# Optimization experiments

Measured on AMD Instinct MI355X. Metric: run time of the kernel, lower is better.

The kernel has to match this reference:

```python
import jax, jax.numpy as jnp
import numpy as np

DIM_MODEL = 512
DIM_HEAD = 64


def setup_inputs() -> dict:
    key = jax.random.key(0)
    ks = jax.random.split(key, 7)
    B, S = 4, 4096
    x = jax.random.normal(ks[0], (B, S, DIM_MODEL), dtype=jnp.float32)
    mask = jnp.ones((B, 1, S), dtype=jnp.int32)
    # torch Linear init: U(-1/sqrt(fan_in), 1/sqrt(fan_in)); stored as (in, out) for x @ W
    bound = 1.0 / np.sqrt(DIM_MODEL)
    Wq = jax.random.uniform(ks[1], (DIM_MODEL, DIM_HEAD), minval=-bound, maxval=bound, dtype=jnp.float32)
    bq = jax.random.uniform(ks[2], (DIM_HEAD,), minval=-bound, maxval=bound, dtype=jnp.float32)
    Wk = jax.random.uniform(ks[3], (DIM_MODEL, DIM_HEAD), minval=-bound, maxval=bound, dtype=jnp.float32)
    bk = jax.random.uniform(ks[4], (DIM_HEAD,), minval=-bound, maxval=bound, dtype=jnp.float32)
    Wv = jax.random.uniform(ks[5], (DIM_MODEL, DIM_HEAD), minval=-bound, maxval=bound, dtype=jnp.float32)
    bv = jax.random.uniform(ks[6], (DIM_HEAD,), minval=-bound, maxval=bound, dtype=jnp.float32)
    return {"x": x, "mask": mask, "Wq": Wq, "bq": bq, "Wk": Wk, "bk": bk, "Wv": Wv, "bv": bv}


def reference(x, mask, Wq, bq, Wk, bk, Wv, bv):
    # single-head QKV projection
    q = x @ Wq + bq  # (B, S, Dh)
    k = x @ Wk + bk
    v = x @ Wv + bv
    dot_scale = jnp.sqrt(jnp.float32(DIM_HEAD))
    # explicit O(S^2) score matrix, softmax over keys
    scores = jnp.einsum("bqd,bkd->bqk", q, k) / dot_scale  # (B, S, S)
    attn = jax.nn.softmax(scores, axis=-1)
    # faithful to source: mask applied AFTER softmax with -inf fill
    attn = jnp.where(mask == 0, jnp.float32(-jnp.inf), attn)
    return jnp.einsum("bqk,bkd->bqd", attn, v)  # (B, S, Dh)
```

## Files before the change

### kernel.cpp

```cpp
#include <hip/hip_runtime.h>
#include <hip/hip_bf16.h>

typedef _Float16 half8v __attribute__((ext_vector_type(8)));
typedef _Float16 half4v __attribute__((ext_vector_type(4)));
typedef _Float16 half2v __attribute__((ext_vector_type(2)));
typedef __fp16   fp16x2 __attribute__((ext_vector_type(2)));
typedef __attribute__((ext_vector_type(4))) float floatx4;

#define LOG2E_OVER_8 0.18033688011112042f


__device__ __forceinline__ void gload_lds16(const void* g, void* l) {
    __builtin_amdgcn_global_load_lds(
        (const __attribute__((address_space(1))) void*)(unsigned long long)g,
        (__attribute__((address_space(3))) void*)(unsigned)(unsigned long long)l,
        16, 0, 0);
}

__global__ __launch_bounds__(256) void wtrans_k(const float* __restrict__ Wq,
                                                const float* __restrict__ Wk,
                                                const float* __restrict__ Wv,
                                                _Float16* __restrict__ Wt) {
    int idx = blockIdx.x * 256 + threadIdx.x;
    int p = idx >> 15, rem = idx & 32767;
    int k = rem >> 6;
    int n = rem & 63;
    const float* W = (p == 0) ? Wq : ((p == 1) ? Wk : Wv);
    int ctg = p * 4 + (n >> 4), m = n & 15;
    int kc = k >> 5, quad = (k >> 3) & 3, j = k & 7;
    Wt[(((ctg << 4) + kc) * 64 + (quad << 4) + m) * 8 + j] = (_Float16)W[k * 64 + n];
}

#define XS_STRIDE 536
__global__ __launch_bounds__(256) void proj_k(const float* __restrict__ x,
                                              const _Float16* __restrict__ Wt,
                                              const float* __restrict__ bq,
                                              const float* __restrict__ bk,
                                              const float* __restrict__ bv,
                                              _Float16* __restrict__ Qh,
                                              _Float16* __restrict__ Kh,
                                              _Float16* __restrict__ Vh) {
    __shared__ _Float16 xs[2][16 * XS_STRIDE];

    int tid = threadIdx.x, l = tid & 63, wv = tid >> 6;
    int m = l & 15, quad = l >> 4;
    int row0 = blockIdx.x * 32;

#pragma unroll
    for (int s = 0; s < 2; s++)
#pragma unroll
        for (int i = 0; i < 8; i++) {
            int idx = tid + i * 256;
            int row = idx >> 7, c4 = idx & 127;
            float4 v = *(const float4*)(x + (row0 + s * 16 + row) * 512 + c4 * 4);
            union { half2v h[2]; uint2 u; } cv;
            cv.h[0][0] = (_Float16)v.x; cv.h[0][1] = (_Float16)v.y;
            cv.h[1][0] = (_Float16)v.z; cv.h[1][1] = (_Float16)v.w;
            *(uint2*)(xs[s] + row * XS_STRIDE + c4 * 4) = cv.u;
        }
    __syncthreads();

    const _Float16* arow0 = xs[0] + m * XS_STRIDE + quad * 8;
    const _Float16* arow1 = xs[1] + m * XS_STRIDE + quad * 8;

    floatx4 acc[2][3];
#pragma unroll
    for (int s = 0; s < 2; s++)
#pragma unroll
        for (int i = 0; i < 3; i++) acc[s][i] = (floatx4)(0.f);

#pragma unroll 4
    for (int kc = 0; kc < 16; kc++) {
        half8v a0 = *(const half8v*)(arow0 + kc * 32);
        half8v a1 = *(const half8v*)(arow1 + kc * 32);
#pragma unroll
        for (int ct = 0; ct < 3; ct++) {
            int ctg = wv * 3 + ct;
            half8v b = *(const half8v*)(Wt + (((ctg << 4) + kc) * 64 + l) * 8);
            acc[0][ct] = __builtin_amdgcn_mfma_f32_16x16x32_f16(a0, b, acc[0][ct], 0, 0, 0);
            acc[1][ct] = __builtin_amdgcn_mfma_f32_16x16x32_f16(a1, b, acc[1][ct], 0, 0, 0);
        }
    }

#pragma unroll
    for (int s = 0; s < 2; s++) {
        int rowb = row0 + s * 16;
#pragma unroll
        for (int ct = 0; ct < 3; ct++) {
            int ctg = wv * 3 + ct;
            int col = ctg * 16 + m;
            float bias = (ctg < 4) ? bq[col] : ((ctg < 8) ? bk[col - 64] : bv[col - 128]);
            if (ctg < 8) {
                _Float16* dst = (ctg < 4) ? Qh : Kh;
                float scl = (ctg < 4) ? LOG2E_OVER_8 : 1.0f;
                int dd = (ctg & 3) * 16 + m;
                int c = dd >> 5, quadQ = (dd >> 3) & 3, j = dd & 7;
#pragma unroll
                for (int r = 0; r < 4; r++) {
                    int row = rowb + quad * 4 + r;
                    int chunk = ((row >> 4) << 1) + c;
                    dst[(chunk * 64 + quadQ * 16 + (row & 15)) * 8 + j] =
                        (_Float16)((acc[s][ct][r] + bias) * scl);
                }
            } else {
                int dt = ctg - 8;
                int t64 = rowb >> 6, ktp = (rowb >> 5) & 1, half = (rowb >> 4) & 1;
                int chunk = t64 * 8 + dt * 2 + ktp;
                union { _Float16 h[4]; unsigned long long u; } pk;
#pragma unroll
                for (int r = 0; r < 4; r++) pk.h[r] = (_Float16)(acc[s][ct][r] + bias);
                *(unsigned long long*)(Vh + (chunk * 64 + quad * 16 + m) * 8 + half * 4) = pk.u;
            }
        }
    }
}

template <int NT>
__global__ __launch_bounds__(256) void attn_k(const _Float16* __restrict__ Qh,
                                              const _Float16* __restrict__ Kh,
                                              const _Float16* __restrict__ Vh,
                                              const int* __restrict__ mask,
                                              _Float16* __restrict__ Np,
                                              float* __restrict__ Dp,
                                              int gshift) {
    __shared__ __align__(16) uint4 stage_lds[2][1024];

    int tid = threadIdx.x, l = tid & 63, wv = tid >> 6;
    int m = l & 15, quad = l >> 4;
    int bid = blockIdx.x;
    int grp = bid & ((1 << gshift) - 1), qblk = bid >> gshift;
    int os = grp >> 2, b = grp & 3;
    int q0 = qblk * 128 + wv * 32;

    const int* maskb = mask + b * 4096 + os * (NT * 64);
    int az = 0;
#pragma unroll
    for (int i = 0; i < NT; i++) az |= (maskb[l + i * 64] == 0);
    const bool hasz = __any(az);

    int qt_g = (b * 4096 + q0) >> 4;
    half8v qf[2][2];
#pragma unroll
    for (int qt = 0; qt < 2; qt++)
#pragma unroll
        for (int c = 0; c < 2; c++)
            qf[qt][c] = *(const half8v*)(Qh + (((qt_g + qt) * 2 + c) * 64 + l) * 8);

    half8v ones8;
#pragma unroll
    for (int i = 0; i < 8; i++) ones8[i] = (_Float16)1.0f;

    int tb0 = (b * 64 + os * NT) * 512;
    const uint4* kh4 = (const uint4*)Kh + tb0;
    const uint4* vh4 = (const uint4*)Vh + tb0;

    floatx4 oacc[2][4];
#pragma unroll
    for (int qt = 0; qt < 2; qt++)
#pragma unroll
        for (int dt = 0; dt < 4; dt++) oacc[qt][dt] = (floatx4)(0.f);
    floatx4 oden[2] = {(floatx4)(0.f), (floatx4)(0.f)};

#pragma unroll
    for (int i = 0; i < 2; i++) {
        int idx = wv * 128 + i * 64 + l;
        gload_lds16(kh4 + idx, &stage_lds[0][0] + idx);
        gload_lds16(vh4 + idx, &stage_lds[0][512] + idx);
    }
    __syncthreads();

#pragma unroll 2
    for (int t = 0; t < NT; t++) {
        int cur = t & 1;
        if (t + 1 < NT) {
            const uint4* ksrc = kh4 + (t + 1) * 512;
            const uint4* vsrc = vh4 + (t + 1) * 512;
            uint4* kb = &stage_lds[cur ^ 1][0];
            uint4* vb = &stage_lds[cur ^ 1][512];
#pragma unroll
            for (int i = 0; i < 2; i++) {
                int idx = wv * 128 + i * 64 + l;
                gload_lds16(ksrc + idx, kb + idx);
                gload_lds16(vsrc + idx, vb + idx);
            }
        }
        const uint4* kt4 = &stage_lds[cur][0];
        const uint4* vt4 = &stage_lds[cur][512];
#pragma unroll
        for (int sp = 0; sp < 2; sp++) {
            union { uint4 u; half8v h; } kk[4];
#pragma unroll
            for (int i = 0; i < 4; i++)
                kk[i].u = kt4[(sp * 4 + i) * 64 + l];
            uint4 vv[4];
#pragma unroll
            for (int dt = 0; dt < 4; dt++)
                vv[dt] = vt4[(dt * 2 + sp) * 64 + l];
            half8v pb8[2];
#pragma unroll
            for (int qt = 0; qt < 2; qt++) {
                union { fp16x2 h2[4]; half8v h8; } pu;
#pragma unroll
                for (int se = 0; se < 2; se++) {
                    floatx4 sf = (floatx4)(0.f);
                    sf = __builtin_amdgcn_mfma_f32_16x16x32_f16(kk[se * 2 + 0].h, qf[qt][0], sf, 0, 0, 0);
                    sf = __builtin_amdgcn_mfma_f32_16x16x32_f16(kk[se * 2 + 1].h, qf[qt][1], sf, 0, 0, 0);
                    float p0 = exp2f(sf[0]), p1 = exp2f(sf[1]);
                    float p2 = exp2f(sf[2]), p3 = exp2f(sf[3]);
                    if (hasz) {
                        int kg = t * 64 + (sp * 2 + se) * 16 + quad * 4;
                        if (maskb[kg + 0] == 0) p0 = -__builtin_inff();
                        if (maskb[kg + 1] == 0) p1 = -__builtin_inff();
                        if (maskb[kg + 2] == 0) p2 = -__builtin_inff();
                        if (maskb[kg + 3] == 0) p3 = -__builtin_inff();
                    }
                    pu.h2[se * 2 + 0] = __builtin_amdgcn_cvt_pkrtz(p0, p1);
                    pu.h2[se * 2 + 1] = __builtin_amdgcn_cvt_pkrtz(p2, p3);
                }
                pb8[qt] = pu.h8;
                oden[qt] = __builtin_amdgcn_mfma_f32_16x16x32_f16(ones8, pb8[qt], oden[qt], 0, 0, 0);
            }
#pragma unroll
            for (int dt = 0; dt < 4; dt++) {
                union { uint4 u; half8v h; } vc; vc.u = vv[dt];
                oacc[0][dt] = __builtin_amdgcn_mfma_f32_16x16x32_f16(vc.h, pb8[0], oacc[0][dt], 0, 0, 0);
                oacc[1][dt] = __builtin_amdgcn_mfma_f32_16x16x32_f16(vc.h, pb8[1], oacc[1][dt], 0, 0, 0);
            }
        }
        __syncthreads();
    }

    float* Tw = (float*)&stage_lds[0][0] + wv * (16 * 68);
    int rowb = os * 16384 + b * 4096 + q0;
#pragma unroll
    for (int qt = 0; qt < 2; qt++) {
        if (l < 16) Dp[rowb + qt * 16 + l] = oden[qt][0];
#pragma unroll
        for (int dt = 0; dt < 4; dt++)
#pragma unroll
            for (int r = 0; r < 4; r++)
                Tw[m * 68 + dt * 16 + quad * 4 + r] = oacc[qt][dt][r];
        __builtin_amdgcn_s_waitcnt(0);
#pragma unroll
        for (int g = 0; g < 4; g++) {
            int idx = g * 64 + l;
            int row = idx >> 4, c4 = (idx & 15) * 4;
            float4 v = *(const float4*)(Tw + row * 68 + c4);
            union { half4v h; unsigned long long u; } pk;
            pk.h[0] = (_Float16)v.x; pk.h[1] = (_Float16)v.y;
            pk.h[2] = (_Float16)v.z; pk.h[3] = (_Float16)v.w;
            *(unsigned long long*)(Np + (size_t)(rowb + qt * 16 + row) * 64 + c4) = pk.u;
        }
        __builtin_amdgcn_s_waitcnt(0);
    }
}

__global__ __launch_bounds__(256) void combine_k(const _Float16* __restrict__ Np,
                                                 const float* __restrict__ Dp,
                                                 float* __restrict__ out,
                                                 int spl) {
    int g4 = blockIdx.x * 256 + threadIdx.x;
    int row = g4 >> 4;
    float4 nu = make_float4(0.f, 0.f, 0.f, 0.f);
    float d = 0.f;
    for (int sp = 0; sp < spl; sp++) {
        union { unsigned long long u; half4v h; } v;
        v.u = *(const unsigned long long*)(Np + ((size_t)sp << 20) + (size_t)g4 * 4);
        nu.x += (float)v.h[0]; nu.y += (float)v.h[1];
        nu.z += (float)v.h[2]; nu.w += (float)v.h[3];
        d += Dp[sp * 16384 + row];
    }
    float inv = 1.0f / d;
    ((float4*)out)[g4] = make_float4(nu.x * inv, nu.y * inv, nu.z * inv, nu.w * inv);
}

extern "C" void kernel_launch(void* const* d_in, const int* in_sizes, int n_in,
                              void* d_out, int out_size, void* d_ws, size_t ws_size,
                              hipStream_t stream) {
    const float* x  = (const float*)d_in[0];
    const int* mask = (const int*)d_in[1];
    const float* Wq = (const float*)d_in[2];
    const float* bq = (const float*)d_in[3];
    const float* Wk = (const float*)d_in[4];
    const float* bk = (const float*)d_in[5];
    const float* Wv = (const float*)d_in[6];
    const float* bv = (const float*)d_in[7];
    float* out = (float*)d_out;

    char* ws = (char*)d_ws;
    _Float16* Wt = (_Float16*)(ws);
    _Float16* Qh = (_Float16*)(ws + 0x40000);
    _Float16* Kh = (_Float16*)(ws + 0x240000);
    _Float16* Vh = (_Float16*)(ws + 0x440000);
    float*    Dp = (float*)(ws + 0x640000);
    _Float16* Np = (_Float16*)(ws + 0x740000);

    wtrans_k<<<384, 256, 0, stream>>>(Wq, Wk, Wv, Wt);
    proj_k<<<512, 256, 0, stream>>>(x, Wt, bq, bk, bv, Qh, Kh, Vh);
    attn_k<8><<<32 * 32, 256, 0, stream>>>(Qh, Kh, Vh, mask, Np, Dp, 5);
    combine_k<<<1024, 256, 0, stream>>>(Np, Dp, out, 8);
}
```

Measured before the change: 133.5 us.

## Read K/V tiles directly from global memory instead of LDS double-buffering

Result: faster. 128.3 us (-3.8%).

```diff
diff --git a/kernel.cpp b/kernel.cpp
--- a/kernel.cpp
+++ b/kernel.cpp
@@ -9,13 +9,6 @@
 
 #define LOG2E_OVER_8 0.18033688011112042f
 
-
-__device__ __forceinline__ void gload_lds16(const void* g, void* l) {
-    __builtin_amdgcn_global_load_lds(
-        (const __attribute__((address_space(1))) void*)(unsigned long long)g,
-        (__attribute__((address_space(3))) void*)(unsigned)(unsigned long long)l,
-        16, 0, 0);
-}
 
 __global__ __launch_bounds__(256) void wtrans_k(const float* __restrict__ Wq,
                                                 const float* __restrict__ Wk,
@@ -116,14 +109,14 @@
 }
 
 template <int NT>
-__global__ __launch_bounds__(256) void attn_k(const _Float16* __restrict__ Qh,
-                                              const _Float16* __restrict__ Kh,
-                                              const _Float16* __restrict__ Vh,
-                                              const int* __restrict__ mask,
-                                              _Float16* __restrict__ Np,
-                                              float* __restrict__ Dp,
-                                              int gshift) {
-    __shared__ __align__(16) uint4 stage_lds[2][1024];
+__global__ __launch_bounds__(256, 4) void attn_k(const _Float16* __restrict__ Qh,
+                                                 const _Float16* __restrict__ Kh,
+                                                 const _Float16* __restrict__ Vh,
+                                                 const int* __restrict__ mask,
+                                                 _Float16* __restrict__ Np,
+                                                 float* __restrict__ Dp,
+                                                 int gshift) {
+    __shared__ float T[4][16 * 68];
 
     int tid = threadIdx.x, l = tid & 63, wv = tid >> 6;
     int m = l & 15, quad = l >> 4;
@@ -161,31 +154,9 @@
         for (int dt = 0; dt < 4; dt++) oacc[qt][dt] = (floatx4)(0.f);
     floatx4 oden[2] = {(floatx4)(0.f), (floatx4)(0.f)};
 
-#pragma unroll
-    for (int i = 0; i < 2; i++) {
-        int idx = wv * 128 + i * 64 + l;
-        gload_lds16(kh4 + idx, &stage_lds[0][0] + idx);
-        gload_lds16(vh4 + idx, &stage_lds[0][512] + idx);
-    }
-    __syncthreads();
-
-#pragma unroll 2
     for (int t = 0; t < NT; t++) {
-        int cur = t & 1;
-        if (t + 1 < NT) {
-            const uint4* ksrc = kh4 + (t + 1) * 512;
-            const uint4* vsrc = vh4 + (t + 1) * 512;
-            uint4* kb = &stage_lds[cur ^ 1][0];
-            uint4* vb = &stage_lds[cur ^ 1][512];
-#pragma unroll
-            for (int i = 0; i < 2; i++) {
-                int idx = wv * 128 + i * 64 + l;
-                gload_lds16(ksrc + idx, kb + idx);
-                gload_lds16(vsrc + idx, vb + idx);
-            }
-        }
-        const uint4* kt4 = &stage_lds[cur][0];
-        const uint4* vt4 = &stage_lds[cur][512];
+        const uint4* kt4 = kh4 + t * 512;
+        const uint4* vt4 = vh4 + t * 512;
 #pragma unroll
         for (int sp = 0; sp < 2; sp++) {
             union { uint4 u; half8v h; } kk[4];
@@ -203,8 +174,10 @@
 #pragma unroll
                 for (int se = 0; se < 2; se++) {
                     floatx4 sf = (floatx4)(0.f);
+                    __builtin_amdgcn_s_setprio(1);
                     sf = __builtin_amdgcn_mfma_f32_16x16x32_f16(kk[se * 2 + 0].h, qf[qt][0], sf, 0, 0, 0);
                     sf = __builtin_amdgcn_mfma_f32_16x16x32_f16(kk[se * 2 + 1].h, qf[qt][1], sf, 0, 0, 0);
+                    __builtin_amdgcn_s_setprio(0);
                     float p0 = exp2f(sf[0]), p1 = exp2f(sf[1]);
                     float p2 = exp2f(sf[2]), p3 = exp2f(sf[3]);
                     if (hasz) {
@@ -218,19 +191,21 @@
                     pu.h2[se * 2 + 1] = __builtin_amdgcn_cvt_pkrtz(p2, p3);
                 }
                 pb8[qt] = pu.h8;
-                oden[qt] = __builtin_amdgcn_mfma_f32_16x16x32_f16(ones8, pb8[qt], oden[qt], 0, 0, 0);
             }
+            __builtin_amdgcn_s_setprio(1);
+            oden[0] = __builtin_amdgcn_mfma_f32_16x16x32_f16(ones8, pb8[0], oden[0], 0, 0, 0);
+            oden[1] = __builtin_amdgcn_mfma_f32_16x16x32_f16(ones8, pb8[1], oden[1], 0, 0, 0);
 #pragma unroll
             for (int dt = 0; dt < 4; dt++) {
                 union { uint4 u; half8v h; } vc; vc.u = vv[dt];
                 oacc[0][dt] = __builtin_amdgcn_mfma_f32_16x16x32_f16(vc.h, pb8[0], oacc[0][dt], 0, 0, 0);
                 oacc[1][dt] = __builtin_amdgcn_mfma_f32_16x16x32_f16(vc.h, pb8[1], oacc[1][dt], 0, 0, 0);
             }
-        }
-        __syncthreads();
-    }
-
-    float* Tw = (float*)&stage_lds[0][0] + wv * (16 * 68);
+            __builtin_amdgcn_s_setprio(0);
+        }
+    }
+
+    float* Tw = &T[wv][0];
     int rowb = os * 16384 + b * 4096 + q0;
 #pragma unroll
     for (int qt = 0; qt < 2; qt++) {
```
